# Optimization experiments

Measured on AMD Instinct MI355X. Metric: run time of the kernel, lower is better.

## Reference

```python
import jax, jax.numpy as jnp
import numpy as np

# 5x5 Gaussian-Laplacian template: kernel = (4*GL) * GL_T, with a2=-a1/8, a3=-a1/16
GL_T = np.zeros((5, 5), np.float32)
GL_T[2, 2] = 1.0
for r, c in [(1, 2), (2, 1), (2, 3), (3, 2)]:
    GL_T[r, c] = -1.0 / 8.0
for r, c in [(0, 2), (1, 1), (1, 3), (2, 0), (2, 4), (3, 1), (3, 3), (4, 2)]:
    GL_T[r, c] = -1.0 / 16.0

SOB0 = np.array([[1, 2, 1], [0, 0, 0], [-1, -2, -1]], np.float32)
SOB45 = np.array([[2, 1, 0], [1, 0, -1], [0, -1, -2]], np.float32)
SOB90 = np.array([[1, 0, -1], [2, 0, -2], [1, 0, -1]], np.float32)
SOB135 = np.array([[0, -1, -2], [1, 0, -1], [2, 1, 0]], np.float32)

# cubic-spaced threshold value table: (10-0)*(i/100)^3, i=0..100
X_VALUES = np.array([10.0 * (i / 100.0) ** 3 for i in range(101)], np.float32)


def conv2d(x, w, stride=1, padding=0):
    return jax.lax.conv_general_dilated(
        x, w, (stride, stride), ((padding, padding), (padding, padding)),
        dimension_numbers=("NCHW", "OIHW", "NCHW"))


def avg_pool(x, k, s, p):
    # PyTorch AvgPool2d default count_include_pad=True -> divide by k*k always
    s_ = jax.lax.reduce_window(x, 0.0, jax.lax.add, (1, 1, k, k), (1, 1, s, s),
                               ((0, 0), (0, 0), (p, p), (p, p)))
    return s_ / float(k * k)


def _gdm(x, gdm_weight, conv_w, bn_gamma, bn_beta, bn_mean, bn_var):
    x = avg_pool(x, 3, 2, 1)                                  # [B,3,H/2,W/2]
    image_a = jnp.mean(x, axis=1, keepdims=True)              # [B,1,h,w]
    y = conv2d(x, conv_w, stride=2, padding=3)                # ConvBN(3,5,7,s2)
    y = (y - bn_mean[None, :, None, None]) * jax.lax.rsqrt(bn_var + 1e-5)[None, :, None, None]
    y = y * bn_gamma[None, :, None, None] + bn_beta[None, :, None, None]
    weight_att = jnp.tanh(jnp.mean(y, axis=(2, 3)))           # [B,5]

    a1 = gdm_weight[0, 0] * 4.0
    kgl = (a1 * jnp.asarray(GL_T))[None, None]                # [1,1,5,5]
    x_GL = jnp.abs(conv2d(image_a, kgl, stride=1, padding=2))
    x_GL = jnp.where(x_GL < 1e-6, 0.0, x_GL)                  # abs/threshold; relu is no-op

    b, _, h, w = x_GL.shape
    x_t = x_GL.reshape(b, 1, -1)                              # [B,1,HW]
    x_max = jnp.max(x_t, axis=-1)                             # [B,1]
    pos = x_t > 0
    all_sum = jnp.sum(pos, axis=-1)                           # [B,1]
    xv = jnp.asarray(X_VALUES)[None, :, None]                 # [1,101,1]
    sub_sum = jnp.sum(pos & (x_t <= xv), axis=-1)             # [B,101]
    percentage = sub_sum / all_sum                            # [B,101] float

    params = jnp.stack([0.2 + 0.05 * weight_att[:, 1],
                        0.4 + 0.05 * weight_att[:, 2],
                        0.6 + 0.05 * weight_att[:, 3],
                        0.8 + 0.05 * weight_att[:, 4]])       # [4,B]
    thr_pct = jnp.sort(params, axis=0).T                      # [B,4]
    z = jnp.abs(percentage[:, None, :] - thr_pct[:, :, None]) # [B,4,101]
    closest = jnp.argmin(z, axis=-1)                          # [B,4]
    threshold = jnp.asarray(X_VALUES)[closest]                # [B,4]

    tmin = jnp.concatenate([jnp.zeros_like(x_max), threshold], axis=-1)[:, :, None]  # [B,5,1]
    tmax = jnp.concatenate([threshold, x_max], axis=-1)[:, :, None]                  # [B,5,1]
    mask = ((x_t > tmin) & (x_t <= tmax)).astype(jnp.float32)                        # [B,5,HW]
    m = mask.reshape(b, 5, h, w)

    m = avg_pool(m, 9, 1, 4)
    m = avg_pool(m, 9, 1, 4)
    m = avg_pool(m, 9, 2, 4)                                  # [B,5,h/2,w/2]
    mf = m.reshape(b, 5, -1)
    mn = jnp.min(mf, axis=2, keepdims=True)
    mx = jnp.max(mf, axis=2, keepdims=True)
    return ((mf - mn) / (mx - mn)).reshape(b, 5, h // 2, w // 2)


def _hge(feat, hge_weight, fc_w, fc_b):
    # directional kernels built from entries of the learned 3x3 weight
    Sob0 = hge_weight[:, :, 0, 0][:, :, None, None]
    Sob45 = hge_weight[:, :, 0, 1][:, :, None, None]
    Sob90 = hge_weight[:, :, 0, 2][:, :, None, None]
    Sob135 = hge_weight[:, :, 1, 0][:, :, None, None]
    a1 = (hge_weight[:, :, 2, 2] * 4.0)[:, :, None, None]
    x_0 = conv2d(feat, Sob0 * jnp.asarray(SOB0), 1, 1)
    x_45 = conv2d(feat, Sob45 * jnp.asarray(SOB45), 1, 1)
    x_90 = conv2d(feat, Sob90 * jnp.asarray(SOB90), 1, 1)
    x_135 = conv2d(feat, Sob135 * jnp.asarray(SOB135), 1, 1)
    x_GL = conv2d(feat, a1 * jnp.asarray(GL_T), 1, 2)
    x_out = jnp.concatenate([x_0, x_45, x_90, x_135, x_GL], axis=1)  # [B,5*C,H,W]
    return conv2d(x_out, fc_w) + fc_b[None, :, None, None]


def setup_inputs() -> dict:
    key = jax.random.key(0)
    ks = jax.random.split(key, 6)
    return {
        "x": jax.random.normal(ks[0], (8, 3, 512, 512), jnp.float32),
        "gdm_weight": jax.random.normal(ks[1], (1, 5), jnp.float32) * 0.5,
        "conv_w": jax.random.normal(ks[2], (5, 3, 7, 7), jnp.float32) * 0.05,
        "bn_gamma": jnp.ones((5,), jnp.float32),
        "bn_beta": jnp.zeros((5,), jnp.float32),
        "bn_mean": jnp.zeros((5,), jnp.float32),
        "bn_var": jnp.ones((5,), jnp.float32),
        "feat": jax.random.normal(ks[3], (8, 64, 128, 128), jnp.float32),
        "hge_weight": jax.random.normal(ks[4], (64, 64, 3, 3), jnp.float32) * 0.05,
        "fc_w": jax.random.normal(ks[5], (64, 320, 1, 1), jnp.float32) * 0.05,
        "fc_b": jnp.zeros((64,), jnp.float32),
    }


def reference(x, gdm_weight, conv_w, bn_gamma, bn_beta, bn_mean, bn_var,
              feat, hge_weight, fc_w, fc_b):
    gdm_out = _gdm(x, gdm_weight, conv_w, bn_gamma, bn_beta, bn_mean, bn_var)
    hge_out = _hge(feat, hge_weight, fc_w, fc_b)
    return gdm_out, hge_out
```

## Files before the change

### kernel.cpp

```cpp
#include <hip/hip_runtime.h>
#include <hip/hip_bf16.h>
#include <math.h>

#define WS_AT    0
#define WS_YSUM  20480
#define WS_XMAX  20520
#define WS_HIST  20528
#define WS_MN    21376
#define WS_MX    21440
#define WS_XP    21504
#define WS_IA    1594368
#define WS_XGL   2118656

#define GDM_OUT  655360

static __device__ __forceinline__ float xv_val(int i) {
    double t = (double)i / 100.0;
    return (float)(10.0 * t * t * t);
}

__global__ __launch_bounds__(256) void k_front(const float* __restrict__ x,
                                               const float* __restrict__ hw,
                                               const float* __restrict__ fcw,
                                               float* __restrict__ xp,
                                               float* __restrict__ ia,
                                               float* __restrict__ At,
                                               float* __restrict__ zr,
                                               unsigned* __restrict__ mnb,
                                               unsigned* __restrict__ mxb) {
    int bid = blockIdx.x;
    if (bid < 2048) {
        int idx = bid * 256 + threadIdx.x;
        int b = idx >> 16; int p = idx & 65535; int oy = p >> 8; int ox = p & 255;
        float cs[3];
#pragma unroll
        for (int c = 0; c < 3; ++c) {
            const float* src = x + (((size_t)(b * 3 + c)) << 18);
            float s = 0.f;
#pragma unroll
            for (int dy = -1; dy <= 1; ++dy) {
                int iy = 2 * oy + dy; if ((unsigned)iy >= 512u) continue;
#pragma unroll
                for (int dx = -1; dx <= 1; ++dx) {
                    int ix = 2 * ox + dx; if ((unsigned)ix >= 512u) continue;
                    s += src[iy * 512 + ix];
                }
            }
            cs[c] = s * (1.f / 9.f);
            xp[(((size_t)(b * 3 + c)) << 16) + p] = cs[c];
        }
        ia[(((size_t)b) << 16) + p] = (cs[0] + cs[1] + cs[2]) * (1.f / 3.f);
    } else if (bid < 2128) {
        int idx = (bid - 2048) * 256 + threadIdx.x;
        int o = idx & 63; int k = idx >> 6;
        int d = k >> 6; int c = k & 63;
        const int goff[5] = {0, 1, 2, 3, 8};
        float s = 0.f;
        for (int m = 0; m < 64; ++m)
            s += fcw[o * 320 + d * 64 + m] * hw[(m * 64 + c) * 9 + goff[d]];
        At[k * 64 + o] = s * ((d == 4) ? 4.f : 1.f);
    } else {
#pragma unroll
        for (int q = 0; q < 4; ++q) {
            int i = threadIdx.x + 256 * q;
            if (i < 864) zr[i] = 0.f;
        }
        if (threadIdx.x < 40) mnb[threadIdx.x] = 0x7f7fffffu;
        else if (threadIdx.x < 80) mxb[threadIdx.x - 40] = 0u;
    }
}

__global__ __launch_bounds__(256) void k_convgl(const float* __restrict__ xp,
                                                const float* __restrict__ w,
                                                float* __restrict__ ysum,
                                                const float* __restrict__ ia,
                                                const float* __restrict__ gdmw,
                                                float* __restrict__ xgl,
                                                int* __restrict__ hist,
                                                unsigned* __restrict__ xmax) {
    __shared__ float wsm[735];
    __shared__ float red[256];
    __shared__ float xv[101];
    __shared__ int sh[102];
    int bid = blockIdx.x;
    int tid = threadIdx.x;
    if (bid < 512) {
        int b = bid >> 6;
        int p = (bid & 63) * 256 + tid;
        int oy = p >> 7, ox = p & 127;
        for (int l = tid; l < 735; l += 256) wsm[l] = w[l];
        __syncthreads();
        float s[5] = {0.f, 0.f, 0.f, 0.f, 0.f};
        for (int ic = 0; ic < 3; ++ic) {
            const float* src = xp + (((size_t)(b * 3 + ic)) << 16);
#pragma unroll
            for (int r = 0; r < 7; ++r) {
                int iy = 2 * oy - 3 + r; if ((unsigned)iy >= 256u) continue;
#pragma unroll
                for (int ss = 0; ss < 7; ++ss) {
                    int ix = 2 * ox - 3 + ss; if ((unsigned)ix >= 256u) continue;
                    float v = src[iy * 256 + ix];
                    int wi = (ic * 7 + r) * 7 + ss;
#pragma unroll
                    for (int co = 0; co < 5; ++co) s[co] = fmaf(wsm[co * 147 + wi], v, s[co]);
                }
            }
        }
#pragma unroll
        for (int co = 0; co < 5; ++co) {
            red[tid] = s[co]; __syncthreads();
            for (int off = 128; off > 0; off >>= 1) {
                if (tid < off) red[tid] += red[tid + off];
                __syncthreads();
            }
            if (tid == 0) atomicAdd(&ysum[b * 5 + co], red[0]);
            __syncthreads();
        }
    } else {
        int idx = bid - 512;
        int b = idx >> 8;
        int p = (idx & 255) * 256 + tid;
        int y = p >> 8, x = p & 255;
        if (tid < 101) xv[tid] = xv_val(tid);
        if (tid < 102) sh[tid] = 0;
        __syncthreads();
        const float* src = ia + (((size_t)b) << 16);
        float a1 = gdmw[0] * 4.f;
        auto rd = [&](int dy, int dx) -> float {
            int iy = y + dy, ix = x + dx;
            if ((unsigned)iy >= 256u || (unsigned)ix >= 256u) return 0.f;
            return src[iy * 256 + ix];
        };
        float acc = rd(0, 0)
            - 0.125f  * (rd(-1, 0) + rd(0, -1) + rd(0, 1) + rd(1, 0))
            - 0.0625f * (rd(-2, 0) + rd(-1, -1) + rd(-1, 1) + rd(0, -2) +
                         rd(0, 2) + rd(1, -1) + rd(1, 1) + rd(2, 0));
        float raw = fabsf(a1 * acc);
        float val = (raw < 1e-6f) ? 0.f : raw;
        xgl[(((size_t)b) << 16) + p] = val;
        if (val > 0.f) {
            int lo = 0, hi = 101;
            while (lo < hi) { int mid = (lo + hi) >> 1; if (val <= xv[mid]) hi = mid; else lo = mid + 1; }
            atomicAdd(&sh[lo], 1);
        }
        red[tid] = val; __syncthreads();
        for (int off = 128; off > 0; off >>= 1) {
            if (tid < off) red[tid] = fmaxf(red[tid], red[tid + off]);
            __syncthreads();
        }
        if (tid == 0) atomicMax(&xmax[b], __float_as_uint(red[0]));
        if (tid < 102 && sh[tid]) atomicAdd(&hist[b * 102 + tid], sh[tid]);
    }
}

__global__ __launch_bounds__(256) void k_pool(const float* __restrict__ xgl,
                                              const float* __restrict__ ysum,
                                              const float* __restrict__ gamma,
                                              const float* __restrict__ beta,
                                              const float* __restrict__ mean,
                                              const float* __restrict__ var,
                                              const int* __restrict__ hist,
                                              const unsigned* __restrict__ xmax,
                                              float* __restrict__ p2,
                                              unsigned* __restrict__ mnb,
                                              unsigned* __restrict__ mxb) {
    int plane = blockIdx.y;
    int r0 = blockIdx.x * 8;
    int b = plane / 5, band = plane - 5 * b;
    __shared__ float mk[39][264];
    __shared__ float p1[31][264];
    __shared__ float sthr[4];
    int tid = threadIdx.x;
    if (tid == 0) {
        float wa[5];
        for (int c = 1; c < 5; ++c) {
            float m = ysum[b * 5 + c] * (1.f / 16384.f);
            wa[c] = tanhf((m - mean[c]) * rsqrtf(var[c] + 1e-5f) * gamma[c] + beta[c]);
        }
        float pr_[4] = {0.2f + 0.05f * wa[1], 0.4f + 0.05f * wa[2],
                        0.6f + 0.05f * wa[3], 0.8f + 0.05f * wa[4]};
        auto sw = [&](int i, int j) { if (pr_[i] > pr_[j]) { float t = pr_[i]; pr_[i] = pr_[j]; pr_[j] = t; } };
        sw(0, 1); sw(2, 3); sw(0, 2); sw(1, 3); sw(1, 2);
        int all = 0;
        for (int i = 0; i <= 101; ++i) all += hist[b * 102 + i];
        float bestz[4] = {1e30f, 1e30f, 1e30f, 1e30f};
        int besti[4] = {0, 0, 0, 0};
        int cum = 0;
        for (int i = 0; i <= 100; ++i) {
            cum += hist[b * 102 + i];
            float pct = (float)cum / (float)all;
            for (int t = 0; t < 4; ++t) {
                float z = fabsf(pct - pr_[t]);
                if (z < bestz[t]) { bestz[t] = z; besti[t] = i; }
            }
        }
        for (int t = 0; t < 4; ++t) sthr[t] = xv_val(besti[t]);
    }
    __syncthreads();
    float tmin = (band == 0) ? 0.f : sthr[band - 1];
    float tmax = (band == 4) ? __uint_as_float(xmax[b]) : sthr[band];
    const float* src = xgl + (((size_t)b) << 16);
    for (int l = tid; l < 39 * 264; l += 256) {
        int i = l / 264, c = l - i * 264;
        int rr = 2 * r0 - 12 + i, cc = c - 4;
        float m = 0.f;
        if ((unsigned)rr < 256u && (unsigned)cc < 256u) {
            float v = src[rr * 256 + cc];
            m = (v > tmin && v <= tmax) ? 1.f : 0.f;
        }
        mk[i][c] = m;
    }
    __syncthreads();
    {
        int c = tid;
        auto hb = [&](int q) -> float {
            float s = 0.f;
#pragma unroll
            for (int k = 0; k < 9; ++k) s += mk[q][c + k];
            return s;
        };
        float w9[9]; float rs = 0.f;
#pragma unroll
        for (int q = 0; q < 8; ++q) { float h = hb(q); w9[q] = h; rs += h; }
#pragma unroll
        for (int pr = 0; pr < 31; ++pr) {
            int q = pr + 8;
            float h = hb(q); w9[q % 9] = h; rs += h;
            float val = rs * (1.f / 81.f);
            int ar = 2 * r0 - 8 + pr;
            if ((unsigned)ar >= 256u) val = 0.f;
            p1[pr][c + 4] = val;
            rs -= w9[pr % 9];
        }
    }
    if (tid < 248) { int i = tid >> 3, p = tid & 7; p1[i][p < 4 ? p : 256 + p] = 0.f; }
    __syncthreads();
    {
        int c = tid;
        auto hb2 = [&](int q) -> float {
            float s = 0.f;
#pragma unroll
            for (int k = 0; k < 9; ++k) s += p1[q][c + k];
            return s;
        };
        float w9[9]; float rs = 0.f;
#pragma unroll
        for (int q = 0; q < 8; ++q) { float h = hb2(q); w9[q] = h; rs += h; }
#pragma unroll
        for (int i2 = 0; i2 < 23; ++i2) {
            int q = i2 + 8;
            float h = hb2(q); w9[q % 9] = h; rs += h;
            float val = rs * (1.f / 81.f);
            int ar = 2 * r0 - 4 + i2;
            if ((unsigned)ar >= 256u) val = 0.f;
            mk[i2][c + 4] = val;
            rs -= w9[i2 % 9];
        }
    }
    if (tid < 184) { int i2 = tid >> 3, p = tid & 7; mk[i2][p < 4 ? p : 256 + p] = 0.f; }
    __syncthreads();
    for (int l = tid; l < 23 * 128; l += 256) {
        int i2 = l >> 7, ox = l & 127;
        float s = 0.f;
#pragma unroll
        for (int k = 0; k < 9; ++k) s += mk[i2][2 * ox + k];
        p1[i2][ox] = s * (1.f / 9.f);
    }
    __syncthreads();
    float vmn = 1e30f, vmx = -1e30f;
    float* dst = p2 + (size_t)plane * 16384;
#pragma unroll
    for (int q = 0; q < 4; ++q) {
        int l = tid + 256 * q;
        int jj = l >> 7, ox = l & 127;
        float s = 0.f;
#pragma unroll
        for (int k = 0; k < 9; ++k) s += p1[2 * jj + k][ox];
        s *= (1.f / 9.f);
        dst[(r0 + jj) * 128 + ox] = s;
        vmn = fminf(vmn, s); vmx = fmaxf(vmx, s);
    }
    __syncthreads();
    float* smn = &mk[0][0];
    float* smx = &mk[1][0];
    smn[tid] = vmn; smx[tid] = vmx; __syncthreads();
    for (int off = 128; off > 0; off >>= 1) {
        if (tid < off) {
            smn[tid] = fminf(smn[tid], smn[tid + off]);
            smx[tid] = fmaxf(smx[tid], smx[tid + off]);
        }
        __syncthreads();
    }
    if (tid == 0) {
        atomicMin(&mnb[plane], __float_as_uint(smn[0]));
        atomicMax(&mxb[plane], __float_as_uint(smx[0]));
    }
}

__global__ __launch_bounds__(512, 2) void k_hge(const float* __restrict__ feat,
                                                const float* __restrict__ At,
                                                const float* __restrict__ fcb,
                                                const float* __restrict__ p2,
                                                const unsigned* __restrict__ mnb,
                                                const unsigned* __restrict__ mxb,
                                                float* __restrict__ gdm,
                                                float* __restrict__ out) {
    int tile = blockIdx.x, b = blockIdx.y;
    int tid = threadIdx.x;
    if (tile == 64) {
        int base = b * 512 + tid;
#pragma unroll
        for (int q = 0; q < 40; ++q) {
            int i4 = base + 4096 * q;
            int idx = i4 * 4;
            int plane = idx >> 14;
            float mn = __uint_as_float(mnb[plane]), mx = __uint_as_float(mxb[plane]);
            float inv = 1.f / (mx - mn);
            float4 v = *(const float4*)&p2[idx];
            float4 o = {(v.x - mn) * inv, (v.y - mn) * inv, (v.z - mn) * inv, (v.w - mn) * inv};
            *(float4*)&gdm[idx] = o;
        }
        return;
    }
    int ty = (tile >> 3) * 16, tx = (tile & 7) * 16;
    int grp = tid >> 8, tg = tid & 255;
    __shared__ float ft[2][20][21];
    __shared__ float tl[2][5][256];
    __shared__ float al[2][2][5][64];
    int og = tg >> 6;
    int pl = tg & 63;
    float acc[4][8];
#pragma unroll
    for (int i = 0; i < 4; ++i)
#pragma unroll
        for (int j = 0; j < 8; ++j) acc[i][j] = 0.f;

    const float* cur[3];
    int str3[3];
    bool ok[3];
#pragma unroll
    for (int j = 0; j < 3; ++j) {
        int l = tid + 512 * j;
        cur[j] = nullptr; str3[j] = 0; ok[j] = false;
        if (l < 800) {
            int ch = (l >= 400); int rem = l - ch * 400;
            int r = rem / 20, cx = rem - r * 20;
            int gy = ty - 2 + r, gx = tx - 2 + cx;
            if ((unsigned)gy < 128u && (unsigned)gx < 128u) {
                cur[j] = feat + (((size_t)(b * 64 + ch)) << 14) + gy * 128 + gx;
                str3[j] = 2 << 14;
                ok[j] = true;
            }
        } else if (l < 1440) {
            int q = l - 800;
            int ch = (q >= 320); int k = q - ch * 320;
            cur[j] = At + (k >> 6) * 4096 + ch * 64 + (k & 63);
            str3[j] = 128;
            ok[j] = true;
        }
    }
    float pr[3];
#pragma unroll
    for (int j = 0; j < 3; ++j) pr[j] = ok[j] ? *cur[j] : 0.f;

    for (int g = 0; g < 32; ++g) {
        int buf = g & 1;
#pragma unroll
        for (int j = 0; j < 3; ++j) {
            int l = tid + 512 * j;
            if (l < 800) {
                int ch = (l >= 400); int rem = l - ch * 400;
                int r = rem / 20, cx = rem - r * 20;
                ft[ch][r][cx] = pr[j];
            } else if (l < 1440) {
                ((float*)al[buf])[l - 800] = pr[j];
            }
        }
        __syncthreads();
        if (g < 31) {
#pragma unroll
            for (int j = 0; j < 3; ++j) {
                if (ok[j]) { cur[j] += str3[j]; pr[j] = *cur[j]; }
            }
        }
        {
            int cy = (tg >> 4) + 2, cx = (tg & 15) + 2;
            int ch = grp;
            float fm2 = ft[ch][cy - 2][cx], f2p = ft[ch][cy + 2][cx];
            float fl2 = ft[ch][cy][cx - 2], fr2 = ft[ch][cy][cx + 2];
            float a  = ft[ch][cy - 1][cx - 1], bq = ft[ch][cy - 1][cx], cc = ft[ch][cy - 1][cx + 1];
            float dd = ft[ch][cy][cx - 1],     ee = ft[ch][cy][cx],     ffv = ft[ch][cy][cx + 1];
            float g_ = ft[ch][cy + 1][cx - 1], h  = ft[ch][cy + 1][cx], i2 = ft[ch][cy + 1][cx + 1];
            tl[ch][0][tg] = (a + 2.f * bq + cc) - (g_ + 2.f * h + i2);
            tl[ch][1][tg] = 2.f * a + bq + dd - ffv - h - 2.f * i2;
            tl[ch][2][tg] = (a - cc) + 2.f * (dd - ffv) + (g_ - i2);
            tl[ch][3][tg] = -bq - 2.f * cc + dd - ffv + 2.f * g_ + h;
            tl[ch][4][tg] = ee - 0.125f * (bq + dd + ffv + h)
                          - 0.0625f * (fm2 + a + cc + fl2 + fr2 + g_ + i2 + f2p);
        }
        __syncthreads();
#pragma unroll
        for (int ch = 0; ch < 2; ++ch) {
#pragma unroll
            for (int d = 0; d < 5; ++d) {
                float4 a0 = *(const float4*)&al[buf][ch][d][grp * 32 + og * 8];
                float4 a1 = *(const float4*)&al[buf][ch][d][grp * 32 + og * 8 + 4];
                float av[8] = {a0.x, a0.y, a0.z, a0.w, a1.x, a1.y, a1.z, a1.w};
#pragma unroll
                for (int pj = 0; pj < 4; ++pj) {
                    float tv = tl[ch][d][pl + 64 * pj];
#pragma unroll
                    for (int oi = 0; oi < 8; ++oi)
                        acc[pj][oi] = fmaf(av[oi], tv, acc[pj][oi]);
                }
            }
        }
    }
#pragma unroll
    for (int oi = 0; oi < 8; ++oi) {
        int o = grp * 32 + og * 8 + oi;
        float bias = fcb[o];
        float* dsto = out + (((size_t)(b * 64 + o)) << 14);
#pragma unroll
        for (int pj = 0; pj < 4; ++pj) {
            int pxl = pl + 64 * pj;
            dsto[(ty + (pxl >> 4)) * 128 + tx + (pxl & 15)] = acc[pj][oi] + bias;
        }
    }
}

extern "C" void kernel_launch(void* const* d_in, const int* in_sizes, int n_in,
                              void* d_out, int out_size, void* d_ws, size_t ws_size,
                              hipStream_t stream) {
    const float* x    = (const float*)d_in[0];
    const float* gdmw = (const float*)d_in[1];
    const float* convw= (const float*)d_in[2];
    const float* bng  = (const float*)d_in[3];
    const float* bnb  = (const float*)d_in[4];
    const float* bnm  = (const float*)d_in[5];
    const float* bnv  = (const float*)d_in[6];
    const float* feat = (const float*)d_in[7];
    const float* hw   = (const float*)d_in[8];
    const float* fcw  = (const float*)d_in[9];
    const float* fcb  = (const float*)d_in[10];
    float* out = (float*)d_out;
    float* ws  = (float*)d_ws;

    float* At   = ws + WS_AT;
    float* ysum = ws + WS_YSUM;
    unsigned* xmax = (unsigned*)(ws + WS_XMAX);
    int* hist   = (int*)(ws + WS_HIST);
    unsigned* mnb = (unsigned*)(ws + WS_MN);
    unsigned* mxb = (unsigned*)(ws + WS_MX);
    float* xp   = ws + WS_XP;
    float* ia   = ws + WS_IA;
    float* xgl  = ws + WS_XGL;
    float* p2   = ws + WS_XP + 20480;

    float* hge = out + GDM_OUT;

    k_front  <<<2129, 256, 0, stream>>>(x, hw, fcw, xp, ia, At, ws + WS_YSUM, mnb, mxb);
    k_convgl <<<2560, 256, 0, stream>>>(xp, convw, ysum, ia, gdmw, xgl, hist, xmax);
    k_pool   <<<dim3(16, 40), 256, 0, stream>>>(xgl, ysum, bng, bnb, bnm, bnv, hist, xmax,
                                                p2, mnb, mxb);
    k_hge    <<<dim3(65, 8), 512, 0, stream>>>(feat, At, fcb, p2, mnb, mxb, out, hge);
}
```

Baseline: 242.1 us.

## Merge HGE compute into conv/GL kernel and split normalization into own kernel

Moves the HGE tile computation out of the last kernel and into the conv/GL kernel as extra blocks, so the heavy HGE work runs alongside the GDM conv and Laplacian work instead of after the pool stage. The conv and GL branches are re-indexed for 512-thread blocks. The final min/max normalization becomes a small standalone kernel. The merged kernel pays for this with higher shared-memory and register use (launch bounds 512,2) in every branch, which can lower occupancy for the light branches.

```diff
diff --git a/kernel.cpp b/kernel.cpp
--- a/kernel.cpp
+++ b/kernel.cpp
@@ -70,25 +70,32 @@
     }
 }
 
-__global__ __launch_bounds__(256) void k_convgl(const float* __restrict__ xp,
-                                                const float* __restrict__ w,
-                                                float* __restrict__ ysum,
-                                                const float* __restrict__ ia,
-                                                const float* __restrict__ gdmw,
-                                                float* __restrict__ xgl,
-                                                int* __restrict__ hist,
-                                                unsigned* __restrict__ xmax) {
+__global__ __launch_bounds__(512, 2) void k_mega(const float* __restrict__ xp,
+                                                 const float* __restrict__ w,
+                                                 float* __restrict__ ysum,
+                                                 const float* __restrict__ ia,
+                                                 const float* __restrict__ gdmw,
+                                                 float* __restrict__ xgl,
+                                                 int* __restrict__ hist,
+                                                 unsigned* __restrict__ xmax,
+                                                 const float* __restrict__ feat,
+                                                 const float* __restrict__ At,
+                                                 const float* __restrict__ fcb,
+                                                 float* __restrict__ out) {
     __shared__ float wsm[735];
-    __shared__ float red[256];
+    __shared__ float red[512];
     __shared__ float xv[101];
     __shared__ int sh[102];
+    __shared__ float ft[2][20][21];
+    __shared__ float tl[2][5][256];
+    __shared__ float al[2][2][5][64];
     int bid = blockIdx.x;
     int tid = threadIdx.x;
-    if (bid < 512) {
-        int b = bid >> 6;
-        int p = (bid & 63) * 256 + tid;
+    if (bid < 256) {
+        int b = bid >> 5;
+        int p = (bid & 31) * 512 + tid;
         int oy = p >> 7, ox = p & 127;
-        for (int l = tid; l < 735; l += 256) wsm[l] = w[l];
+        for (int l = tid; l < 735; l += 512) wsm[l] = w[l];
         __syncthreads();
         float s[5] = {0.f, 0.f, 0.f, 0.f, 0.f};
         for (int ic = 0; ic < 3; ++ic) {
@@ -109,17 +116,17 @@
 #pragma unroll
         for (int co = 0; co < 5; ++co) {
             red[tid] = s[co]; __syncthreads();
-            for (int off = 128; off > 0; off >>= 1) {
+            for (int off = 256; off > 0; off >>= 1) {
                 if (tid < off) red[tid] += red[tid + off];
                 __syncthreads();
             }
             if (tid == 0) atomicAdd(&ysum[b * 5 + co], red[0]);
             __syncthreads();
         }
-    } else {
-        int idx = bid - 512;
-        int b = idx >> 8;
-        int p = (idx & 255) * 256 + tid;
+    } else if (bid < 1280) {
+        int idx = bid - 256;
+        int b = idx >> 7;
+        int p = (idx & 127) * 512 + tid;
         int y = p >> 8, x = p & 255;
         if (tid < 101) xv[tid] = xv_val(tid);
         if (tid < 102) sh[tid] = 0;
@@ -144,12 +151,117 @@
             atomicAdd(&sh[lo], 1);
         }
         red[tid] = val; __syncthreads();
-        for (int off = 128; off > 0; off >>= 1) {
+        for (int off = 256; off > 0; off >>= 1) {
             if (tid < off) red[tid] = fmaxf(red[tid], red[tid + off]);
             __syncthreads();
         }
         if (tid == 0) atomicMax(&xmax[b], __float_as_uint(red[0]));
         if (tid < 102 && sh[tid]) atomicAdd(&hist[b * 102 + tid], sh[tid]);
+    } else {
+        int hb = bid - 1280;
+        int tile = hb & 63, b = hb >> 6;
+        int ty = (tile >> 3) * 16, tx = (tile & 7) * 16;
+        int grp = tid >> 8, tg = tid & 255;
+        int og = tg >> 6;
+        int pl = tg & 63;
+        float acc[4][8];
+#pragma unroll
+        for (int i = 0; i < 4; ++i)
+#pragma unroll
+            for (int j = 0; j < 8; ++j) acc[i][j] = 0.f;
+
+        const float* cur[3];
+        int str3[3];
+        bool ok[3];
+#pragma unroll
+        for (int j = 0; j < 3; ++j) {
+            int l = tid + 512 * j;
+            cur[j] = nullptr; str3[j] = 0; ok[j] = false;
+            if (l < 800) {
+                int ch = (l >= 400); int rem = l - ch * 400;
+                int r = rem / 20, cx = rem - r * 20;
+                int gy = ty - 2 + r, gx = tx - 2 + cx;
+                if ((unsigned)gy < 128u && (unsigned)gx < 128u) {
+                    cur[j] = feat + (((size_t)(b * 64 + ch)) << 14) + gy * 128 + gx;
+                    str3[j] = 2 << 14;
+                    ok[j] = true;
+                }
+            } else if (l < 1440) {
+                int q = l - 800;
+                int ch = (q >= 320); int k = q - ch * 320;
+                cur[j] = At + (k >> 6) * 4096 + ch * 64 + (k & 63);
+                str3[j] = 128;
+                ok[j] = true;
+            }
+        }
+        float pr[3];
+#pragma unroll
+        for (int j = 0; j < 3; ++j) pr[j] = ok[j] ? *cur[j] : 0.f;
+
+        for (int g = 0; g < 32; ++g) {
+            int buf = g & 1;
+#pragma unroll
+            for (int j = 0; j < 3; ++j) {
+                int l = tid + 512 * j;
+                if (l < 800) {
+                    int ch = (l >= 400); int rem = l - ch * 400;
+                    int r = rem / 20, cx = rem - r * 20;
+                    ft[ch][r][cx] = pr[j];
+                } else if (l < 1440) {
+                    ((float*)al[buf])[l - 800] = pr[j];
+                }
+            }
+            __syncthreads();
+            if (g < 31) {
+#pragma unroll
+                for (int j = 0; j < 3; ++j) {
+                    if (ok[j]) { cur[j] += str3[j]; pr[j] = *cur[j]; }
+                }
+            }
+            {
+                int cy = (tg >> 4) + 2, cx = (tg & 15) + 2;
+                int ch = grp;
+                float fm2 = ft[ch][cy - 2][cx], f2p = ft[ch][cy + 2][cx];
+                float fl2 = ft[ch][cy][cx - 2], fr2 = ft[ch][cy][cx + 2];
+                float a  = ft[ch][cy - 1][cx - 1], bq = ft[ch][cy - 1][cx], cc = ft[ch][cy - 1][cx + 1];
+                float dd = ft[ch][cy][cx - 1],     ee = ft[ch][cy][cx],     ffv = ft[ch][cy][cx + 1];
+                float g_ = ft[ch][cy + 1][cx - 1], h  = ft[ch][cy + 1][cx], i2 = ft[ch][cy + 1][cx + 1];
+                tl[ch][0][tg] = (a + 2.f * bq + cc) - (g_ + 2.f * h + i2);
+                tl[ch][1][tg] = 2.f * a + bq + dd - ffv - h - 2.f * i2;
+                tl[ch][2][tg] = (a - cc) + 2.f * (dd - ffv) + (g_ - i2);
+                tl[ch][3][tg] = -bq - 2.f * cc + dd - ffv + 2.f * g_ + h;
+                tl[ch][4][tg] = ee - 0.125f * (bq + dd + ffv + h)
+                              - 0.0625f * (fm2 + a + cc + fl2 + fr2 + g_ + i2 + f2p);
+            }
+            __syncthreads();
+#pragma unroll
+            for (int ch = 0; ch < 2; ++ch) {
+#pragma unroll
+                for (int d = 0; d < 5; ++d) {
+                    float4 a0 = *(const float4*)&al[buf][ch][d][grp * 32 + og * 8];
+                    float4 a1 = *(const float4*)&al[buf][ch][d][grp * 32 + og * 8 + 4];
+                    float av[8] = {a0.x, a0.y, a0.z, a0.w, a1.x, a1.y, a1.z, a1.w};
+#pragma unroll
+                    for (int pj = 0; pj < 4; ++pj) {
+                        float tv = tl[ch][d][pl + 64 * pj];
+#pragma unroll
+                        for (int oi = 0; oi < 8; ++oi)
+                            acc[pj][oi] = fmaf(av[oi], tv, acc[pj][oi]);
+                    }
+                }
+            }
+        }
+#pragma unroll
+        for (int oi = 0; oi < 8; ++oi) {
+            int o = grp * 32 + og * 8 + oi;
+            float bias = fcb[o];
+            float* dsto = out + (((size_t)(b * 64 + o)) << 14);
+#pragma unroll
+            for (int pj = 0; pj < 4; ++pj) {
+                int pxl = pl + 64 * pj;
+                dsto[(ty + (pxl >> 4)) * 128 + tx + (pxl & 15)] = acc[pj][oi] + bias;
+            }
+        }
     }
 }
 
@@ -297,136 +409,18 @@
     }
 }
 
-__global__ __launch_bounds__(512, 2) void k_hge(const float* __restrict__ feat,
-                                                const float* __restrict__ At,
-                                                const float* __restrict__ fcb,
-                                                const float* __restrict__ p2,
-                                                const unsigned* __restrict__ mnb,
-                                                const unsigned* __restrict__ mxb,
-                                                float* __restrict__ gdm,
-                                                float* __restrict__ out) {
-    int tile = blockIdx.x, b = blockIdx.y;
-    int tid = threadIdx.x;
-    if (tile == 64) {
-        int base = b * 512 + tid;
-#pragma unroll
-        for (int q = 0; q < 40; ++q) {
-            int i4 = base + 4096 * q;
-            int idx = i4 * 4;
-            int plane = idx >> 14;
-            float mn = __uint_as_float(mnb[plane]), mx = __uint_as_float(mxb[plane]);
-            float inv = 1.f / (mx - mn);
-            float4 v = *(const float4*)&p2[idx];
-            float4 o = {(v.x - mn) * inv, (v.y - mn) * inv, (v.z - mn) * inv, (v.w - mn) * inv};
-            *(float4*)&gdm[idx] = o;
-        }
-        return;
-    }
-    int ty = (tile >> 3) * 16, tx = (tile & 7) * 16;
-    int grp = tid >> 8, tg = tid & 255;
-    __shared__ float ft[2][20][21];
-    __shared__ float tl[2][5][256];
-    __shared__ float al[2][2][5][64];
-    int og = tg >> 6;
-    int pl = tg & 63;
-    float acc[4][8];
-#pragma unroll
-    for (int i = 0; i < 4; ++i)
-#pragma unroll
-        for (int j = 0; j < 8; ++j) acc[i][j] = 0.f;
-
-    const float* cur[3];
-    int str3[3];
-    bool ok[3];
-#pragma unroll
-    for (int j = 0; j < 3; ++j) {
-        int l = tid + 512 * j;
-        cur[j] = nullptr; str3[j] = 0; ok[j] = false;
-        if (l < 800) {
-            int ch = (l >= 400); int rem = l - ch * 400;
-            int r = rem / 20, cx = rem - r * 20;
-            int gy = ty - 2 + r, gx = tx - 2 + cx;
-            if ((unsigned)gy < 128u && (unsigned)gx < 128u) {
-                cur[j] = feat + (((size_t)(b * 64 + ch)) << 14) + gy * 128 + gx;
-                str3[j] = 2 << 14;
-                ok[j] = true;
-            }
-        } else if (l < 1440) {
-            int q = l - 800;
-            int ch = (q >= 320); int k = q - ch * 320;
-            cur[j] = At + (k >> 6) * 4096 + ch * 64 + (k & 63);
-            str3[j] = 128;
-            ok[j] = true;
-        }
-    }
-    float pr[3];
-#pragma unroll
-    for (int j = 0; j < 3; ++j) pr[j] = ok[j] ? *cur[j] : 0.f;
-
-    for (int g = 0; g < 32; ++g) {
-        int buf = g & 1;
-#pragma unroll
-        for (int j = 0; j < 3; ++j) {
-            int l = tid + 512 * j;
-            if (l < 800) {
-                int ch = (l >= 400); int rem = l - ch * 400;
-                int r = rem / 20, cx = rem - r * 20;
-                ft[ch][r][cx] = pr[j];
-            } else if (l < 1440) {
-                ((float*)al[buf])[l - 800] = pr[j];
-            }
-        }
-        __syncthreads();
-        if (g < 31) {
-#pragma unroll
-            for (int j = 0; j < 3; ++j) {
-                if (ok[j]) { cur[j] += str3[j]; pr[j] = *cur[j]; }
-            }
-        }
-        {
-            int cy = (tg >> 4) + 2, cx = (tg & 15) + 2;
-            int ch = grp;
-            float fm2 = ft[ch][cy - 2][cx], f2p = ft[ch][cy + 2][cx];
-            float fl2 = ft[ch][cy][cx - 2], fr2 = ft[ch][cy][cx + 2];
-            float a  = ft[ch][cy - 1][cx - 1], bq = ft[ch][cy - 1][cx], cc = ft[ch][cy - 1][cx + 1];
-            float dd = ft[ch][cy][cx - 1],     ee = ft[ch][cy][cx],     ffv = ft[ch][cy][cx + 1];
-            float g_ = ft[ch][cy + 1][cx - 1], h  = ft[ch][cy + 1][cx], i2 = ft[ch][cy + 1][cx + 1];
-            tl[ch][0][tg] = (a + 2.f * bq + cc) - (g_ + 2.f * h + i2);
-            tl[ch][1][tg] = 2.f * a + bq + dd - ffv - h - 2.f * i2;
-            tl[ch][2][tg] = (a - cc) + 2.f * (dd - ffv) + (g_ - i2);
-            tl[ch][3][tg] = -bq - 2.f * cc + dd - ffv + 2.f * g_ + h;
-            tl[ch][4][tg] = ee - 0.125f * (bq + dd + ffv + h)
-                          - 0.0625f * (fm2 + a + cc + fl2 + fr2 + g_ + i2 + f2p);
-        }
-        __syncthreads();
-#pragma unroll
-        for (int ch = 0; ch < 2; ++ch) {
-#pragma unroll
-            for (int d = 0; d < 5; ++d) {
-                float4 a0 = *(const float4*)&al[buf][ch][d][grp * 32 + og * 8];
-                float4 a1 = *(const float4*)&al[buf][ch][d][grp * 32 + og * 8 + 4];
-                float av[8] = {a0.x, a0.y, a0.z, a0.w, a1.x, a1.y, a1.z, a1.w};
-#pragma unroll
-                for (int pj = 0; pj < 4; ++pj) {
-                    float tv = tl[ch][d][pl + 64 * pj];
-#pragma unroll
-                    for (int oi = 0; oi < 8; ++oi)
-                        acc[pj][oi] = fmaf(av[oi], tv, acc[pj][oi]);
-                }
-            }
-        }
-    }
-#pragma unroll
-    for (int oi = 0; oi < 8; ++oi) {
-        int o = grp * 32 + og * 8 + oi;
-        float bias = fcb[o];
-        float* dsto = out + (((size_t)(b * 64 + o)) << 14);
-#pragma unroll
-        for (int pj = 0; pj < 4; ++pj) {
-            int pxl = pl + 64 * pj;
-            dsto[(ty + (pxl >> 4)) * 128 + tx + (pxl & 15)] = acc[pj][oi] + bias;
-        }
-    }
+__global__ __launch_bounds__(256) void k_norm(const float* __restrict__ in,
+                                              const unsigned* __restrict__ mnb,
+                                              const unsigned* __restrict__ mxb,
+                                              float* __restrict__ gdm) {
+    int i4 = blockIdx.x * 256 + threadIdx.x;
+    int idx = i4 * 4;
+    int plane = idx >> 14;
+    float mn = __uint_as_float(mnb[plane]), mx = __uint_as_float(mxb[plane]);
+    float inv = 1.f / (mx - mn);
+    float4 v = *(const float4*)&in[idx];
+    float4 o = {(v.x - mn) * inv, (v.y - mn) * inv, (v.z - mn) * inv, (v.w - mn) * inv};
+    *(float4*)&gdm[idx] = o;
 }
 
 extern "C" void kernel_launch(void* const* d_in, const int* in_sizes, int n_in,
@@ -459,9 +453,10 @@
 
     float* hge = out + GDM_OUT;
 
-    k_front  <<<2129, 256, 0, stream>>>(x, hw, fcw, xp, ia, At, ws + WS_YSUM, mnb, mxb);
-    k_convgl <<<2560, 256, 0, stream>>>(xp, convw, ysum, ia, gdmw, xgl, hist, xmax);
-    k_pool   <<<dim3(16, 40), 256, 0, stream>>>(xgl, ysum, bng, bnb, bnm, bnv, hist, xmax,
-                                                p2, mnb, mxb);
-    k_hge    <<<dim3(65, 8), 512, 0, stream>>>(feat, At, fcb, p2, mnb, mxb, out, hge);
-}
+    k_front <<<2129, 256, 0, stream>>>(x, hw, fcw, xp, ia, At, ws + WS_YSUM, mnb, mxb);
+    k_mega  <<<1792, 512, 0, stream>>>(xp, convw, ysum, ia, gdmw, xgl, hist, xmax,
+                                       feat, At, fcb, hge);
+    k_pool  <<<dim3(16, 40), 256, 0, stream>>>(xgl, ysum, bng, bnb, bnm, bnv, hist, xmax,
+                                               p2, mnb, mxb);
+    k_norm  <<<640, 256, 0, stream>>>(p2, mnb, mxb, out);
+}
```

Result: faster. 214.2 us (-11.5%).
